# Kernel optimization log

Hardware: AMD Instinct MI355X
Metric: run time of the kernel (lower is better)

## Reference

```python
import jax, jax.numpy as jnp
import numpy as np

N = 2048      # feature_num (nodes/sensors)
T = 5         # timd_num (window length)
D = 64        # embed_dim
TOPK = 21     # topk + 1 (includes self, cos(i,i)=1)
B = 32        # batch
EPS = 1e-5
NEG_SLOPE = 0.2


def setup_inputs() -> dict:
    key = jax.random.key(0)
    ks = jax.random.split(key, 9)
    s = 1.0 / np.sqrt(D)
    return {
        "x": jax.random.normal(ks[0], (B, N, T), jnp.float32),
        "emb": jax.random.normal(ks[1], (N, D), jnp.float32) * s,      # embedding table
        "W": jax.random.normal(ks[2], (D, T), jnp.float32) * (1.0 / np.sqrt(T)),  # GNN lin weight
        "Wb": jax.random.normal(ks[3], (D,), jnp.float32) * 0.01,       # GNN lin bias
        "a_src": jax.random.normal(ks[4], (2 * D,), jnp.float32) * s,   # attention vec (source half)
        "a_dst": jax.random.normal(ks[5], (2 * D,), jnp.float32) * s,   # attention vec (dest half)
        "gamma": jnp.ones((D,), jnp.float32),                            # BatchNorm1d weight
        "beta": jnp.zeros((D,), jnp.float32),                            # BatchNorm1d bias
        "fc_w": jax.random.normal(ks[6], (1, D), jnp.float32) * s,      # fc weight
        "fc_b": jnp.zeros((1,), jnp.float32),                            # fc bias
    }


def reference(x, emb, W, Wb, a_src, a_dst, gamma, beta, fc_w, fc_b):
    # --- cosine-sim topk graph build ---
    norm = jnp.linalg.norm(emb, axis=-1)                    # [N]
    cos = (emb @ emb.T) / (norm[:, None] * norm[None, :])   # [N,N]
    _, idx = jax.lax.top_k(cos, TOPK)                       # [N,TOPK]
    # scatter one-hot adjacency (vectorized, no per-row loop)
    adj = jnp.zeros((N, N), x.dtype).at[jnp.arange(N)[:, None], idx].set(1.0)
    # --- GNN: GDN-style attention message passing ---
    h = jnp.einsum('bnt,dt->bnd', x, W) + Wb                # [B,N,D]
    g = jnp.concatenate([h, jnp.broadcast_to(emb, h.shape)], axis=-1)  # [B,N,2D]
    e_src = g @ a_src                                       # [B,N]
    e_dst = g @ a_dst                                       # [B,N]
    e = jax.nn.leaky_relu(e_src[:, :, None] + e_dst[:, None, :], NEG_SLOPE)  # [B,N,N]
    e = jnp.where(adj > 0, e, jnp.float32(-1e9))
    alpha = jax.nn.softmax(e, axis=-1)                      # [B,N,N], rows sum to 1 over TOPK nbrs
    z = jax.nn.relu(jnp.einsum('bij,bjd->bid', alpha, h))   # [B,N,D]
    # --- output head: z * emb, BN over channels, relu, fc ---
    out = z * emb                                           # [B,N,D]
    mean = out.mean(axis=(0, 1))                            # BN1d stats over (batch, nodes)
    var = out.var(axis=(0, 1))
    out = (out - mean) * jax.lax.rsqrt(var + EPS) * gamma + beta
    out = jax.nn.relu(out)
    out = out @ fc_w.T + fc_b                               # [B,N,1]
    return out.reshape(-1, N)                               # [B,N]
```

## Files before the change

kernel.cpp:

```cpp
#include <hip/hip_runtime.h>
#include <math.h>

#define N_NODES 2048
#define T_WIN 5
#define D_EMB 64
#define TOPK 21
#define B_BATCH 32
#define BN_TOTAL (B_BATCH * N_NODES)
#define EPS_BN 1e-5f
#define NEG_SLOPE 0.2f
#define STATS_STRIDE 16

typedef unsigned long long u64;

__device__ __forceinline__ float wave_sum(float v) {
#pragma unroll
    for (int off = 32; off > 0; off >>= 1) v += __shfl_xor(v, off, 64);
    return v;
}

__device__ __forceinline__ u64 max64(u64 a, u64 b) { return a > b ? a : b; }
__device__ __forceinline__ u64 min64(u64 a, u64 b) { return a < b ? a : b; }

__device__ __forceinline__ u64 bitonic_sort64_desc(u64 key, int lane) {
#pragma unroll
    for (int k = 2; k <= 64; k <<= 1) {
#pragma unroll
        for (int j = k >> 1; j >= 1; j >>= 1) {
            u64 pk = __shfl_xor(key, j, 64);
            bool dirDesc = ((lane & k) == 0);
            bool keepMax = (((lane & j) == 0) == dirDesc);
            key = keepMax ? max64(key, pk) : min64(key, pk);
        }
    }
    return key;
}

__device__ __forceinline__ u64 bitonic_merge_top64(u64 a, u64 b, int lane) {
    u64 br = __shfl(b, 63 - lane, 64);
    u64 c = max64(a, br);
#pragma unroll
    for (int j = 32; j >= 1; j >>= 1) {
        u64 pk = __shfl_xor(c, j, 64);
        bool keepMax = ((lane & j) == 0);
        c = keepMax ? max64(c, pk) : min64(c, pk);
    }
    return c;
}

__global__ __launch_bounds__(256) void k_edge(
    const float* __restrict__ x, const float* __restrict__ W,
    const float* __restrict__ Wb, const float* __restrict__ a_src,
    const float* __restrict__ a_dst, const float* __restrict__ emb,
    float* __restrict__ es2T, float* __restrict__ ed2T,
    float* __restrict__ norms, float* __restrict__ stats,
    float* __restrict__ stats2) {
    if (blockIdx.x < 2) {
        float* p = blockIdx.x ? stats2 : stats;
        ((float4*)p)[threadIdx.x] = make_float4(0.f, 0.f, 0.f, 0.f);
    }
    int wid = threadIdx.x >> 6, lane = threadIdx.x & 63;
    int gw = blockIdx.x * 4 + wid;
    const float* wp = W + lane * T_WIN;
    float w0 = wp[0], w1 = wp[1], w2 = wp[2], w3 = wp[3], w4 = wp[4];
    float bias = Wb[lane];
    float as = a_src[lane], asE = a_src[D_EMB + lane];
    float ad = a_dst[lane], adE = a_dst[D_EMB + lane];

    for (int node = gw; node < BN_TOTAL; node += 8192) {
        int n = node & (N_NODES - 1);
        const float* xp = x + (size_t)node * T_WIN;
        float hv = bias + xp[0] * w0 + xp[1] * w1 + xp[2] * w2 + xp[3] * w3 + xp[4] * w4;
        float e = emb[n * D_EMB + lane];
        if (node < N_NODES) {
            float s2 = wave_sum(e * e);
            if (lane == 0) norms[node] = sqrtf(s2);
        }
        float es = wave_sum(hv * as + e * asE);
        float ed = wave_sum(hv * ad + e * adE);
        if (lane == 0) {
            es2T[node] = es;
            ed2T[node] = ed;
        }
    }
}

__global__ __launch_bounds__(256) void k_gram(
    const float* __restrict__ emb, const float* __restrict__ norms,
    float* __restrict__ cosM) {
    __shared__ __align__(16) float As[64][68];
    __shared__ __align__(16) float Bs[64][68];
    int t = threadIdx.x;
    int g = blockIdx.x;
    int a = (int)((sqrtf(8.f * g + 1.f) - 1.f) * 0.5f);
    while ((a + 1) * (a + 2) / 2 <= g) a++;
    while (a * (a + 1) / 2 > g) a--;
    int bq = g - a * (a + 1) / 2;
    int i0 = a * 64, j0 = bq * 64;

    {
        int r = t >> 2, c0 = t & 3;
        const float4* srcA = (const float4*)(emb + (size_t)(i0 + r) * D_EMB);
        const float4* srcB = (const float4*)(emb + (size_t)(j0 + r) * D_EMB);
#pragma unroll
        for (int k = 0; k < 4; k++) {
            int f4 = c0 + 4 * k;
            float4 v = srcA[f4];
            int d = 4 * f4;
            As[d][r] = v.x; As[d + 1][r] = v.y; As[d + 2][r] = v.z; As[d + 3][r] = v.w;
            float4 w = srcB[f4];
            Bs[d][r] = w.x; Bs[d + 1][r] = w.y; Bs[d + 2][r] = w.z; Bs[d + 3][r] = w.w;
        }
    }
    __syncthreads();

    int ti = t & 15, tj = t >> 4;
    float acc[4][4] = {};
#pragma unroll
    for (int d = 0; d < 64; d++) {
        float4 av = *(const float4*)&As[d][4 * ti];
        float4 bv = *(const float4*)&Bs[d][4 * tj];
        acc[0][0] += av.x * bv.x; acc[0][1] += av.x * bv.y; acc[0][2] += av.x * bv.z; acc[0][3] += av.x * bv.w;
        acc[1][0] += av.y * bv.x; acc[1][1] += av.y * bv.y; acc[1][2] += av.y * bv.z; acc[1][3] += av.y * bv.w;
        acc[2][0] += av.z * bv.x; acc[2][1] += av.z * bv.y; acc[2][2] += av.z * bv.z; acc[2][3] += av.z * bv.w;
        acc[3][0] += av.w * bv.x; acc[3][1] += av.w * bv.y; acc[3][2] += av.w * bv.z; acc[3][3] += av.w * bv.w;
    }

    float nis[4] = {norms[i0 + 4 * ti], norms[i0 + 4 * ti + 1],
                    norms[i0 + 4 * ti + 2], norms[i0 + 4 * ti + 3]};
    float njs[4] = {norms[j0 + 4 * tj], norms[j0 + 4 * tj + 1],
                    norms[j0 + 4 * tj + 2], norms[j0 + 4 * tj + 3]};
#pragma unroll
    for (int r = 0; r < 4; r++) {
        float4 o;
        o.x = acc[r][0] / (nis[r] * njs[0]);
        o.y = acc[r][1] / (nis[r] * njs[1]);
        o.z = acc[r][2] / (nis[r] * njs[2]);
        o.w = acc[r][3] / (nis[r] * njs[3]);
        int i = i0 + 4 * ti + r;
        *(float4*)(cosM + (size_t)i * N_NODES + j0 + 4 * tj) = o;
        cosM[(size_t)(j0 + 4 * tj + 0) * N_NODES + i] = o.x;
        cosM[(size_t)(j0 + 4 * tj + 1) * N_NODES + i] = o.y;
        cosM[(size_t)(j0 + 4 * tj + 2) * N_NODES + i] = o.z;
        cosM[(size_t)(j0 + 4 * tj + 3) * N_NODES + i] = o.w;
    }
}

__global__ __launch_bounds__(256) void k_select(
    const float* __restrict__ cosM, int* __restrict__ idxT) {
    __shared__ u64 candbuf[4][128];
    int tid = threadIdx.x;
    int wid = tid >> 6, lane = tid & 63;
    int i = blockIdx.x * 4 + wid;
    const float* row = cosM + (size_t)i * N_NODES;
    u64* buf = candbuf[wid];

    u64 a = 0;
    u64 t = 0;
    int cnt = 0;
    float vcur = row[lane];

#pragma unroll 1
    for (int c = 0; c < N_NODES / 64; c++) {
        int j = c * 64 + lane;
        float v = vcur;
        if (c < N_NODES / 64 - 1) vcur = row[j + 64];
        unsigned u = __float_as_uint(v);
        u = (u & 0x80000000u) ? ~u : (u | 0x80000000u);
        u64 key = ((u64)u << 32) | (unsigned)(~j);
        unsigned long long ball = __ballot(key > t);
        if (ball) {
            int ofs = __popcll(ball & ((1ull << lane) - 1ull));
            if (key > t) buf[cnt + ofs] = key;
            cnt += (int)__popcll(ball);
            if (cnt >= 64) {
                u64 nk = buf[lane];
                nk = bitonic_sort64_desc(nk, lane);
                a = bitonic_merge_top64(a, nk, lane);
                t = __shfl(a, 20, 64);
                int rem = cnt - 64;
                u64 mv = (lane < rem) ? buf[64 + lane] : 0;
                if (lane < rem) buf[lane] = mv;
                cnt = rem;
            }
        }
    }
    while (cnt > 0) {
        int take = cnt < 64 ? cnt : 64;
        u64 nk = (lane < take) ? buf[lane] : 0;
        nk = bitonic_sort64_desc(nk, lane);
        a = bitonic_merge_top64(a, nk, lane);
        t = __shfl(a, 20, 64);
        int rem = cnt - take;
        u64 mv = (lane < rem) ? buf[take + lane] : 0;
        if (lane < rem) buf[lane] = mv;
        cnt = rem;
    }

    if (lane < TOPK) idxT[lane * N_NODES + i] = (int)(~(unsigned)a);
}

__global__ __launch_bounds__(256) void k_alpha(
    const int* __restrict__ idxT, const float* __restrict__ es2T,
    const float* __restrict__ ed2T, float* __restrict__ alphaT) {
    __shared__ float sed[N_NODES];
    int g = blockIdx.x;
    int b = g & 31;
    int i0 = (g >> 5) * 256;
    int t = threadIdx.x;

    {
        const float4* src = (const float4*)(ed2T + (size_t)b * N_NODES);
        float4* dst = (float4*)sed;
#pragma unroll
        for (int q = 0; q < 2; q++) dst[t + 256 * q] = src[t + 256 * q];
    }
    __syncthreads();

    int i = i0 + t;
    float es = es2T[(size_t)b * N_NODES + i];
    float ev[TOPK];
    float m = -3e38f;
#pragma unroll
    for (int k = 0; k < TOPK; k++) {
        int jk = idxT[k * N_NODES + i];
        float e = es + sed[jk];
        e = e > 0.f ? e : NEG_SLOPE * e;
        ev[k] = e;
        m = fmaxf(m, e);
    }
    float s = 0.f;
#pragma unroll
    for (int k = 0; k < TOPK; k++) {
        ev[k] = __expf(ev[k] - m);
        s += ev[k];
    }
    float inv = 1.0f / s;
#pragma unroll
    for (int k = 0; k < TOPK; k++)
        alphaT[((size_t)b * TOPK + k) * N_NODES + i] = ev[k] * inv;
}

__global__ __launch_bounds__(256, 2) void k_msg(
    const float* __restrict__ x, const float* __restrict__ W,
    const float* __restrict__ Wb, const int* __restrict__ idxT,
    const float* __restrict__ alphaT, const float* __restrict__ emb,
    float* __restrict__ obufT, float* __restrict__ stats,
    float* __restrict__ stats2) {
    __shared__ float hts[N_NODES][6];
    __shared__ float sred[2][4][4];

    int g = blockIdx.x;
    int b = (g & 7) + 8 * ((g >> 3) & 3);
    int c = g >> 5;
    int d0 = c * 4;
    int t = threadIdx.x;
    int wid = t >> 6, lane = t & 63;

    float wc[4][T_WIN], wb4[4];
#pragma unroll
    for (int q = 0; q < 4; q++) {
        wb4[q] = Wb[d0 + q];
#pragma unroll
        for (int tt = 0; tt < T_WIN; tt++) wc[q][tt] = W[(d0 + q) * T_WIN + tt];
    }
    const float* xb = x + (size_t)b * N_NODES * T_WIN;
#pragma unroll
    for (int r = 0; r < 8; r++) {
        int row = t + 256 * r;
        const float* xr = xb + row * T_WIN;
        float x0 = xr[0], x1 = xr[1], x2 = xr[2], x3 = xr[3], x4 = xr[4];
        float h0 = wb4[0] + x0 * wc[0][0] + x1 * wc[0][1] + x2 * wc[0][2] + x3 * wc[0][3] + x4 * wc[0][4];
        float h1 = wb4[1] + x0 * wc[1][0] + x1 * wc[1][1] + x2 * wc[1][2] + x3 * wc[1][3] + x4 * wc[1][4];
        float h2 = wb4[2] + x0 * wc[2][0] + x1 * wc[2][1] + x2 * wc[2][2] + x3 * wc[2][3] + x4 * wc[2][4];
        float h3 = wb4[3] + x0 * wc[3][0] + x1 * wc[3][1] + x2 * wc[3][2] + x3 * wc[3][3] + x4 * wc[3][4];
        *(float2*)&hts[row][0] = make_float2(h0, h1);
        *(float2*)&hts[row][2] = make_float2(h2, h3);
    }
    __syncthreads();

    float sacc[4] = {0.f, 0.f, 0.f, 0.f};
    float sacc2[4] = {0.f, 0.f, 0.f, 0.f};
    const float* aT = alphaT + (size_t)b * TOPK * N_NODES;
#pragma unroll 1
    for (int r = 0; r < 8; r++) {
        int i = 256 * r + t;
        float4 z = make_float4(0.f, 0.f, 0.f, 0.f);
#pragma unroll
        for (int k = 0; k < TOPK; k++) {
            int jk = idxT[k * N_NODES + i];
            float a = aT[(size_t)k * N_NODES + i];
            float2 h01 = *(const float2*)&hts[jk][0];
            float2 h23 = *(const float2*)&hts[jk][2];
            z.x = fmaf(a, h01.x, z.x);
            z.y = fmaf(a, h01.y, z.y);
            z.z = fmaf(a, h23.x, z.z);
            z.w = fmaf(a, h23.y, z.w);
        }
        float4 e4 = *(const float4*)(emb + (size_t)i * D_EMB + d0);
        float4 o;
        o.x = fmaxf(z.x, 0.f) * e4.x;
        o.y = fmaxf(z.y, 0.f) * e4.y;
        o.z = fmaxf(z.z, 0.f) * e4.z;
        o.w = fmaxf(z.w, 0.f) * e4.w;
        ((float4*)obufT)[((size_t)c * B_BATCH + b) * N_NODES + i] = o;
        sacc[0] += o.x; sacc[1] += o.y; sacc[2] += o.z; sacc[3] += o.w;
        sacc2[0] += o.x * o.x; sacc2[1] += o.y * o.y;
        sacc2[2] += o.z * o.z; sacc2[3] += o.w * o.w;
    }

#pragma unroll
    for (int q = 0; q < 4; q++) {
        sacc[q] = wave_sum(sacc[q]);
        sacc2[q] = wave_sum(sacc2[q]);
    }
    if (lane == 0) {
#pragma unroll
        for (int q = 0; q < 4; q++) {
            sred[0][wid][q] = sacc[q];
            sred[1][wid][q] = sacc2[q];
        }
    }
    __syncthreads();
    if (t < 8) {
        int q = t & 3, which = t >> 2;
        float v = sred[which][0][q] + sred[which][1][q] + sred[which][2][q] + sred[which][3][q];
        float* dst = which ? stats2 : stats;
        atomicAdd(&dst[(d0 + q) * STATS_STRIDE], v);
    }
}

__global__ __launch_bounds__(256) void k_out(
    const float* __restrict__ obufT, const float* __restrict__ stats,
    const float* __restrict__ stats2, const float* __restrict__ gamma,
    const float* __restrict__ beta, const float* __restrict__ fc_w,
    const float* __restrict__ fc_b, float* __restrict__ out) {
    int t = threadIdx.x;
    int wid = t >> 6, lane = t & 63;
    int nloc = lane >> 4, c = lane & 15;
    const float invM = 1.0f / (float)BN_TOTAL;

    float mean[4], inv[4], g4[4], bt4[4], fw4[4];
#pragma unroll
    for (int q = 0; q < 4; q++) {
        int d = 4 * c + q;
        float mn = stats[d * STATS_STRIDE] * invM;
        float var = stats2[d * STATS_STRIDE] * invM - mn * mn;
        mean[q] = mn;
        inv[q] = rsqrtf(var + EPS_BN);
        g4[q] = gamma[d]; bt4[q] = beta[d]; fw4[q] = fc_w[d];
    }
    float fb = fc_b[0];

#pragma unroll 1
    for (int r = 0; r < 8; r++) {
        int nd = blockIdx.x * 128 + r * 16 + wid * 4 + nloc;
        int b = nd >> 11, n = nd & (N_NODES - 1);
        float4 o = ((const float4*)obufT)[((size_t)c * B_BATCH + b) * N_NODES + n];
        float p = 0.f;
        float v;
        v = fmaxf((o.x - mean[0]) * inv[0] * g4[0] + bt4[0], 0.f); p = fmaf(v, fw4[0], p);
        v = fmaxf((o.y - mean[1]) * inv[1] * g4[1] + bt4[1], 0.f); p = fmaf(v, fw4[1], p);
        v = fmaxf((o.z - mean[2]) * inv[2] * g4[2] + bt4[2], 0.f); p = fmaf(v, fw4[2], p);
        v = fmaxf((o.w - mean[3]) * inv[3] * g4[3] + bt4[3], 0.f); p = fmaf(v, fw4[3], p);
#pragma unroll
        for (int off = 1; off <= 8; off <<= 1) p += __shfl_xor(p, off, 64);
        if (c == 0) out[nd] = p + fb;
    }
}

extern "C" void kernel_launch(void* const* d_in, const int* in_sizes, int n_in,
                              void* d_out, int out_size, void* d_ws, size_t ws_size,
                              hipStream_t stream) {
    const float* x     = (const float*)d_in[0];
    const float* emb   = (const float*)d_in[1];
    const float* W     = (const float*)d_in[2];
    const float* Wb    = (const float*)d_in[3];
    const float* a_src = (const float*)d_in[4];
    const float* a_dst = (const float*)d_in[5];
    const float* gamma = (const float*)d_in[6];
    const float* beta  = (const float*)d_in[7];
    const float* fc_w  = (const float*)d_in[8];
    const float* fc_b  = (const float*)d_in[9];
    float* out = (float*)d_out;

    char* ws = (char*)d_ws;
    float* stats  = (float*)(ws + 0);
    float* stats2 = (float*)(ws + 4096);
    int*   idxT   = (int*)  (ws + 8192);
    float* norms  = (float*)(ws + 180224);
    float* es2T   = (float*)(ws + 188416);
    float* ed2T   = (float*)(ws + 450560);
    float* alphaT = (float*)(ws + 712704);
    float* cosM   = (float*)(ws + 6217728);
    float* obufT  = cosM;

    k_edge<<<2048, 256, 0, stream>>>(x, W, Wb, a_src, a_dst, emb,
                                     es2T, ed2T, norms, stats, stats2);
    k_gram<<<528, 256, 0, stream>>>(emb, norms, cosM);
    k_select<<<N_NODES / 4, 256, 0, stream>>>(cosM, idxT);
    k_alpha<<<256, 256, 0, stream>>>(idxT, es2T, ed2T, alphaT);
    k_msg<<<512, 256, 0, stream>>>(x, W, Wb, idxT, alphaT, emb, obufT, stats, stats2);
    k_out<<<512, 256, 0, stream>>>(obufT, stats, stats2, gamma, beta, fc_w, fc_b, out);
}
```

Measured before the change: 151.5 us.

## Fuse attention softmax into message-passing kernel, drop alpha buffer

Removes the separate k_alpha kernel and recomputes the edge scores and softmax inside k_msg, using a shared-memory copy of ed2T per batch. This eliminates the write and re-read of the B*TOPK*N alpha array plus one kernel launch. Each of the 16 channel-group blocks per batch now redundantly recomputes the softmax, and the h table stride changes from 6 to 5 floats with scalar LDS reads instead of float2.

```diff
diff --git a/kernel.cpp b/kernel.cpp
--- a/kernel.cpp
+++ b/kernel.cpp
@@ -200,54 +200,14 @@
     if (lane < TOPK) idxT[lane * N_NODES + i] = (int)(~(unsigned)a);
 }
 
-__global__ __launch_bounds__(256) void k_alpha(
-    const int* __restrict__ idxT, const float* __restrict__ es2T,
-    const float* __restrict__ ed2T, float* __restrict__ alphaT) {
-    __shared__ float sed[N_NODES];
-    int g = blockIdx.x;
-    int b = g & 31;
-    int i0 = (g >> 5) * 256;
-    int t = threadIdx.x;
-
-    {
-        const float4* src = (const float4*)(ed2T + (size_t)b * N_NODES);
-        float4* dst = (float4*)sed;
-#pragma unroll
-        for (int q = 0; q < 2; q++) dst[t + 256 * q] = src[t + 256 * q];
-    }
-    __syncthreads();
-
-    int i = i0 + t;
-    float es = es2T[(size_t)b * N_NODES + i];
-    float ev[TOPK];
-    float m = -3e38f;
-#pragma unroll
-    for (int k = 0; k < TOPK; k++) {
-        int jk = idxT[k * N_NODES + i];
-        float e = es + sed[jk];
-        e = e > 0.f ? e : NEG_SLOPE * e;
-        ev[k] = e;
-        m = fmaxf(m, e);
-    }
-    float s = 0.f;
-#pragma unroll
-    for (int k = 0; k < TOPK; k++) {
-        ev[k] = __expf(ev[k] - m);
-        s += ev[k];
-    }
-    float inv = 1.0f / s;
-#pragma unroll
-    for (int k = 0; k < TOPK; k++)
-        alphaT[((size_t)b * TOPK + k) * N_NODES + i] = ev[k] * inv;
-}
-
 __global__ __launch_bounds__(256, 2) void k_msg(
     const float* __restrict__ x, const float* __restrict__ W,
     const float* __restrict__ Wb, const int* __restrict__ idxT,
-    const float* __restrict__ alphaT, const float* __restrict__ emb,
-    float* __restrict__ obufT, float* __restrict__ stats,
-    float* __restrict__ stats2) {
-    __shared__ float hts[N_NODES][6];
+    const float* __restrict__ es2T, const float* __restrict__ ed2T,
+    const float* __restrict__ emb, float* __restrict__ obufT,
+    float* __restrict__ stats, float* __restrict__ stats2) {
+    __shared__ float hts[N_NODES * 5];
+    __shared__ float sed[N_NODES];
     __shared__ float sred[2][4][4];
 
     int g = blockIdx.x;
@@ -257,6 +217,13 @@
     int t = threadIdx.x;
     int wid = t >> 6, lane = t & 63;
 
+    {
+        const float4* src = (const float4*)(ed2T + (size_t)b * N_NODES);
+        float4* dst = (float4*)sed;
+        dst[t] = src[t];
+        dst[t + 256] = src[t + 256];
+    }
+
     float wc[4][T_WIN], wb4[4];
 #pragma unroll
     for (int q = 0; q < 4; q++) {
@@ -270,32 +237,49 @@
         int row = t + 256 * r;
         const float* xr = xb + row * T_WIN;
         float x0 = xr[0], x1 = xr[1], x2 = xr[2], x3 = xr[3], x4 = xr[4];
-        float h0 = wb4[0] + x0 * wc[0][0] + x1 * wc[0][1] + x2 * wc[0][2] + x3 * wc[0][3] + x4 * wc[0][4];
-        float h1 = wb4[1] + x0 * wc[1][0] + x1 * wc[1][1] + x2 * wc[1][2] + x3 * wc[1][3] + x4 * wc[1][4];
-        float h2 = wb4[2] + x0 * wc[2][0] + x1 * wc[2][1] + x2 * wc[2][2] + x3 * wc[2][3] + x4 * wc[2][4];
-        float h3 = wb4[3] + x0 * wc[3][0] + x1 * wc[3][1] + x2 * wc[3][2] + x3 * wc[3][3] + x4 * wc[3][4];
-        *(float2*)&hts[row][0] = make_float2(h0, h1);
-        *(float2*)&hts[row][2] = make_float2(h2, h3);
+        float* hp = &hts[row * 5];
+        hp[0] = wb4[0] + x0 * wc[0][0] + x1 * wc[0][1] + x2 * wc[0][2] + x3 * wc[0][3] + x4 * wc[0][4];
+        hp[1] = wb4[1] + x0 * wc[1][0] + x1 * wc[1][1] + x2 * wc[1][2] + x3 * wc[1][3] + x4 * wc[1][4];
+        hp[2] = wb4[2] + x0 * wc[2][0] + x1 * wc[2][1] + x2 * wc[2][2] + x3 * wc[2][3] + x4 * wc[2][4];
+        hp[3] = wb4[3] + x0 * wc[3][0] + x1 * wc[3][1] + x2 * wc[3][2] + x3 * wc[3][3] + x4 * wc[3][4];
     }
     __syncthreads();
 
     float sacc[4] = {0.f, 0.f, 0.f, 0.f};
     float sacc2[4] = {0.f, 0.f, 0.f, 0.f};
-    const float* aT = alphaT + (size_t)b * TOPK * N_NODES;
+    const float* esb = es2T + (size_t)b * N_NODES;
 #pragma unroll 1
     for (int r = 0; r < 8; r++) {
         int i = 256 * r + t;
+        float es = esb[i];
+        int jk[TOPK];
+        float ev[TOPK];
+        float m = -3e38f;
+#pragma unroll
+        for (int k = 0; k < TOPK; k++) {
+            jk[k] = idxT[k * N_NODES + i];
+            float e = es + sed[jk[k]];
+            e = e > 0.f ? e : NEG_SLOPE * e;
+            ev[k] = e;
+            m = fmaxf(m, e);
+        }
+        float s = 0.f;
+#pragma unroll
+        for (int k = 0; k < TOPK; k++) {
+            ev[k] = __expf(ev[k] - m);
+            s += ev[k];
+        }
+        float inv = 1.0f / s;
+
         float4 z = make_float4(0.f, 0.f, 0.f, 0.f);
 #pragma unroll
         for (int k = 0; k < TOPK; k++) {
-            int jk = idxT[k * N_NODES + i];
-            float a = aT[(size_t)k * N_NODES + i];
-            float2 h01 = *(const float2*)&hts[jk][0];
-            float2 h23 = *(const float2*)&hts[jk][2];
-            z.x = fmaf(a, h01.x, z.x);
-            z.y = fmaf(a, h01.y, z.y);
-            z.z = fmaf(a, h23.x, z.z);
-            z.w = fmaf(a, h23.y, z.w);
+            float aw = ev[k] * inv;
+            const float* hp = &hts[jk[k] * 5];
+            z.x = fmaf(aw, hp[0], z.x);
+            z.y = fmaf(aw, hp[1], z.y);
+            z.z = fmaf(aw, hp[2], z.z);
+            z.w = fmaf(aw, hp[3], z.w);
         }
         float4 e4 = *(const float4*)(emb + (size_t)i * D_EMB + d0);
         float4 o;
@@ -391,15 +375,14 @@
     float* norms  = (float*)(ws + 180224);
     float* es2T   = (float*)(ws + 188416);
     float* ed2T   = (float*)(ws + 450560);
-    float* alphaT = (float*)(ws + 712704);
-    float* cosM   = (float*)(ws + 6217728);
+    float* cosM   = (float*)(ws + 712704);
     float* obufT  = cosM;
 
     k_edge<<<2048, 256, 0, stream>>>(x, W, Wb, a_src, a_dst, emb,
                                      es2T, ed2T, norms, stats, stats2);
     k_gram<<<528, 256, 0, stream>>>(emb, norms, cosM);
     k_select<<<N_NODES / 4, 256, 0, stream>>>(cosM, idxT);
-    k_alpha<<<256, 256, 0, stream>>>(idxT, es2T, ed2T, alphaT);
-    k_msg<<<512, 256, 0, stream>>>(x, W, Wb, idxT, alphaT, emb, obufT, stats, stats2);
+    k_msg<<<512, 256, 0, stream>>>(x, W, Wb, idxT, es2T, ed2T, emb,
+                                   obufT, stats, stats2);
     k_out<<<512, 256, 0, stream>>>(obufT, stats, stats2, gamma, beta, fc_w, fc_b, out);
 }
```

After: 156.0 us. 2.9% more time.
